# Performance work log

Hardware: AMD Instinct MI355X
Metric: run time of the kernel (lower is better)

Reference implementation:

```python
import jax, jax.numpy as jnp
import numpy as np

D_MODEL = 768
NUM_HEADS = 12
D_K = D_MODEL // NUM_HEADS
B, S = 2, 2048


def setup_inputs() -> dict:
    key = jax.random.key(0)
    ks = jax.random.split(key, 7)
    scale = 1.0 / np.sqrt(D_MODEL)
    return {
        "query": jax.random.normal(ks[0], (B, S, D_MODEL), jnp.float32),
        "key_in": jax.random.normal(ks[1], (B, S, D_MODEL), jnp.float32),
        "value": jax.random.normal(ks[2], (B, S, D_MODEL), jnp.float32),
        # nn.Linear weights are [out, in]; y = x @ W.T
        "Wq": jax.random.normal(ks[3], (D_MODEL, D_MODEL), jnp.float32) * scale,
        "Wk": jax.random.normal(ks[4], (D_MODEL, D_MODEL), jnp.float32) * scale,
        "Wv": jax.random.normal(ks[5], (D_MODEL, D_MODEL), jnp.float32) * scale,
        "Wo": jax.random.normal(ks[6], (D_MODEL, D_MODEL), jnp.float32) * scale,
    }


def _split_heads(x):
    b, s, _ = x.shape
    return x.reshape(b, s, NUM_HEADS, D_K).transpose(0, 2, 1, 3)  # [B,H,S,Dk]


def reference(query, key_in, value, Wq, Wk, Wv, Wo):
    Q = _split_heads(query @ Wq.T)
    K = _split_heads(key_in @ Wk.T)
    V = _split_heads(value @ Wv.T)
    scores = jnp.einsum("bhqd,bhkd->bhqk", Q, K) / jnp.sqrt(jnp.float32(D_K))
    attn = jax.nn.softmax(scores, axis=-1)
    ctx = jnp.einsum("bhqk,bhkd->bhqd", attn, V)  # [B,H,S,Dk]
    ctx = ctx.transpose(0, 2, 1, 3).reshape(query.shape[0], query.shape[1], D_MODEL)
    return ctx @ Wo.T
```

## Files before the change

### kernel.cpp

```cpp
#include <hip/hip_runtime.h>
#include <hip/hip_bf16.h>


typedef __bf16 bf16x8 __attribute__((ext_vector_type(8)));
typedef float f32x4 __attribute__((ext_vector_type(4)));
typedef unsigned short u16;
typedef unsigned int u32;
typedef u16 u16x8 __attribute__((ext_vector_type(8)));
typedef u16 u16x4 __attribute__((ext_vector_type(4)));

#define SEQ 2048
#define DM  768
#define NH  12
#define DK  64
#define NBH 24
#define MTOT 4096
#define NEL 3145728
#define NWL 589824

__device__ __forceinline__ u16 f2b(float v) {
  __bf16 t = (__bf16)v;
  return __builtin_bit_cast(u16, t);
}

__device__ __forceinline__ void gl_lds16(const u16* g, u16* l) {
  __builtin_amdgcn_global_load_lds(
      (const __attribute__((address_space(1))) void*)g,
      (__attribute__((address_space(3))) void*)l, 16, 0, 0);
}

__device__ __forceinline__ int pos32(int k) {
  return (k < 16) ? (((k >> 2) << 3) + (k & 3))
                  : ((((k & 15) >> 2) << 3) + (k & 3) + 4);
}


__global__ __launch_bounds__(256) void to_bf16(
    const float* __restrict__ s0, const float* __restrict__ s1, const float* __restrict__ s2,
    const float* __restrict__ s3, const float* __restrict__ s4, const float* __restrict__ s5,
    const float* __restrict__ s6, u16* __restrict__ Xb, u16* __restrict__ Wb)
{
  size_t c = (size_t)blockIdx.x * 256 + threadIdx.x;
  const float* src;
  u16* dst;
  if (c < 1179648) {
    int seg = (int)(c / 393216);
    size_t off = (c % 393216) * 8;
    src = (seg == 0 ? s0 : seg == 1 ? s1 : s2) + off;
    dst = Xb + (size_t)seg * NEL + off;
  } else {
    size_t c2 = c - 1179648;
    int seg = (int)(c2 / 73728);
    size_t off = (c2 % 73728) * 8;
    src = (seg == 0 ? s3 : seg == 1 ? s4 : seg == 2 ? s5 : s6) + off;
    dst = Wb + (size_t)seg * NWL + off;
  }
  float4 f0 = *(const float4*)(src);
  float4 f1 = *(const float4*)(src + 4);
  u16x8 o;
  o[0] = f2b(f0.x); o[1] = f2b(f0.y); o[2] = f2b(f0.z); o[3] = f2b(f0.w);
  o[4] = f2b(f1.x); o[5] = f2b(f1.y); o[6] = f2b(f1.z); o[7] = f2b(f1.w);
  *(u16x8*)dst = o;
}

__device__ __forceinline__ void gemm2_core(
    const u16* __restrict__ X, const u16* __restrict__ W, void* __restrict__ Y,
    int m0, int n0, int mode, u16* As, u16* Bs)
{
  const int tid  = threadIdx.x;
  const int lane = tid & 63, w = tid >> 6;
  const int l15  = lane & 15, quad = lane >> 4;
  const int wm   = (w & 1) * 64, wn = (w >> 1) * 64;

  f32x4 acc[4][4] = {};

  for (int k0 = 0; k0 < DM; k0 += 64) {
    __syncthreads();
#pragma unroll
    for (int i = 0; i < 4; i++) {
      int c = (w * 4 + i) * 64 + lane;
      int row = c >> 3, c8 = c & 7;
      int g8 = c8 ^ (row & 7);
      gl_lds16(X + (size_t)(m0 + row) * DM + k0 + g8 * 8, As + c * 8);
      gl_lds16(W + (size_t)(n0 + row) * DM + k0 + g8 * 8, Bs + c * 8);
    }
    __syncthreads();
#pragma unroll
    for (int dk = 0; dk < 2; dk++) {
      bf16x8 af[4], bf[4];
      int ph = ((dk * 4 + quad) ^ (l15 & 7)) * 8;
#pragma unroll
      for (int t = 0; t < 4; t++) {
        af[t] = *(const bf16x8*)(&As[(wm + t * 16 + l15) * 64 + ph]);
        bf[t] = *(const bf16x8*)(&Bs[(wn + t * 16 + l15) * 64 + ph]);
      }
#pragma unroll
      for (int mt = 0; mt < 4; mt++)
#pragma unroll
        for (int nt = 0; nt < 4; nt++)
          acc[mt][nt] = __builtin_amdgcn_mfma_f32_16x16x32_bf16(af[mt], bf[nt], acc[mt][nt], 0, 0, 0);
    }
  }

  if (mode == 2) {
    float* O = (float*)Y;
#pragma unroll
    for (int mt = 0; mt < 4; mt++) {
      int mg = m0 + wm + mt * 16 + quad * 4;
#pragma unroll
      for (int nt = 0; nt < 4; nt++) {
        int j = n0 + wn + nt * 16 + l15;
#pragma unroll
        for (int r = 0; r < 4; r++)
          O[(size_t)(mg + r) * DM + j] = acc[mt][nt][r];
      }
    }
  } else if (mode == 1) {
    u16* O = (u16*)Y;
#pragma unroll
    for (int mt = 0; mt < 4; mt++) {
      int mg = m0 + wm + mt * 16 + quad * 4;
      int b = mg >> 11, s = mg & 2047;
      int sp = (s & ~31) | pos32(s & 31);
#pragma unroll
      for (int nt = 0; nt < 4; nt++) {
        int j = n0 + wn + nt * 16 + l15;
        int h = j >> 6, d = j & 63;
        u16x4 o;
#pragma unroll
        for (int r = 0; r < 4; r++) o[r] = f2b(acc[mt][nt][r]);
        *(u16x4*)&O[((size_t)(b * NH + h) * DK + d) * SEQ + sp] = o;
      }
    }
  } else {
    u16* O = (u16*)Y;
    u16* T = As;
#pragma unroll
    for (int h2 = 0; h2 < 2; h2++) {
      __syncthreads();
      if ((w & 1) == h2) {
#pragma unroll
        for (int mt = 0; mt < 4; mt++)
#pragma unroll
          for (int nt = 0; nt < 4; nt++)
#pragma unroll
            for (int r = 0; r < 4; r++)
              T[(mt * 16 + quad * 4 + r) * 128 + wn + nt * 16 + l15] = f2b(acc[mt][nt][r]);
      }
      __syncthreads();
#pragma unroll
      for (int i = 0; i < 4; i++) {
        int c = i * 256 + tid;
        int row = c >> 4, ch = c & 15;
        u16x8 val = *(const u16x8*)&T[row * 128 + ch * 8];
        int m = m0 + h2 * 64 + row;
        int j = n0 + ch * 8;
        int hh = j >> 6, d = j & 63;
        int b = m >> 11, s = m & 2047;
        *(u16x8*)&O[((size_t)(b * NH + hh) * SEQ + s) * DK + d] = val;
      }
    }
  }
}

__global__ __launch_bounds__(256) void qkv2(
    const u16* __restrict__ Xb, const u16* __restrict__ Wb,
    u16* __restrict__ Qhm, u16* __restrict__ Khm, u16* __restrict__ Vt)
{
  __shared__ __align__(16) u16 As[128 * 64];
  __shared__ __align__(16) u16 Bs[128 * 64];
  int mat = blockIdx.z;
  const u16* X = Xb + (size_t)mat * NEL;
  const u16* W = Wb + (size_t)mat * NWL;
  void* Y = (mat == 0) ? (void*)Qhm : (mat == 1) ? (void*)Khm : (void*)Vt;
  gemm2_core(X, W, Y, blockIdx.y * 128, blockIdx.x * 128, (mat == 2) ? 1 : 0, As, Bs);
}

__global__ __launch_bounds__(256) void bt2(
    const u16* __restrict__ Ctx, const u16* __restrict__ Wob, float* __restrict__ Y)
{
  __shared__ __align__(16) u16 As[128 * 64];
  __shared__ __align__(16) u16 Bs[128 * 64];
  gemm2_core(Ctx, Wob, Y, blockIdx.y * 128, blockIdx.x * 128, 2, As, Bs);
}

__global__ __launch_bounds__(256) void attn2(
    const u16* __restrict__ Qh, const u16* __restrict__ Kh,
    const u16* __restrict__ Vt, u16* __restrict__ ctx)
{
  __shared__ __align__(16) u16 smem[128 * 64 + 64 * 128];
  __shared__ float Ls[64];
  u16* Ks = smem;
  u16* Vs = smem + 128 * 64;

  const int tid  = threadIdx.x;
  const int lane = tid & 63, w = tid >> 6;
  const int l15  = lane & 15, quad = lane >> 4;
  const int qh = w & 1, kh = w >> 1;
  const int qt = blockIdx.x, bh = blockIdx.y;
  const int b = bh / NH, h = bh % NH;

  const u16* Qb = Qh + (size_t)bh * SEQ * DK;
  const u16* Kb = Kh + (size_t)bh * SEQ * DK;
  const u16* Vb = Vt + (size_t)bh * DK * SEQ;
  const int q0 = qt * 64 + qh * 32;

  bf16x8 qf[2][2];
#pragma unroll
  for (int QT = 0; QT < 2; QT++)
#pragma unroll
    for (int dk = 0; dk < 2; dk++)
      qf[QT][dk] = *(const bf16x8*)&Qb[(size_t)(q0 + QT * 16 + l15) * DK + dk * 32 + quad * 8];

  float lpart[2] = {0.f, 0.f};
  f32x4 oacc[4][2] = {};

  for (int kt = 0; kt < SEQ; kt += 128) {
    __syncthreads();
#pragma unroll
    for (int i = 0; i < 4; i++) {
      int c = (w * 4 + i) * 64 + lane;
      int row = c >> 3, c8 = c & 7;
      gl_lds16(Kb + (size_t)(kt + row) * DK + (c8 ^ (row & 7)) * 8, Ks + c * 8);
    }
#pragma unroll
    for (int i = 0; i < 4; i++) {
      int c = (w * 4 + i) * 64 + lane;
      int d = c >> 4, c16 = c & 15;
      gl_lds16(Vb + (size_t)d * SEQ + kt + (c16 ^ (d & 15)) * 8, Vs + c * 8);
    }
    __syncthreads();

    f32x4 sc[4][2] = {};
#pragma unroll
    for (int MT = 0; MT < 4; MT++) {
      int row = kh * 64 + MT * 16 + l15;
#pragma unroll
      for (int dk = 0; dk < 2; dk++) {
        bf16x8 kf = *(const bf16x8*)&Ks[row * 64 + ((dk * 4 + quad) ^ (l15 & 7)) * 8];
        sc[MT][0] = __builtin_amdgcn_mfma_f32_16x16x32_bf16(kf, qf[0][dk], sc[MT][0], 0, 0, 0);
        sc[MT][1] = __builtin_amdgcn_mfma_f32_16x16x32_bf16(kf, qf[1][dk], sc[MT][1], 0, 0, 0);
      }
    }

    bf16x8 pf[2][2];
#pragma unroll
    for (int QT = 0; QT < 2; QT++)
#pragma unroll
      for (int kk = 0; kk < 2; kk++)
#pragma unroll
        for (int j = 0; j < 8; j++) {
          float s = sc[kk * 2 + (j >> 2)][QT][j & 3] * 0.125f;
          float p = __expf(fminf(s, 30.0f));
          lpart[QT] += p;
          pf[kk][QT][j] = (__bf16)p;
        }

#pragma unroll
    for (int kk = 0; kk < 2; kk++) {
      int cL = kh * 8 + kk * 4 + quad;
#pragma unroll
      for (int DT = 0; DT < 4; DT++) {
        int d = DT * 16 + l15;
        bf16x8 vf = *(const bf16x8*)&Vs[d * 128 + (cL ^ (d & 15)) * 8];
        oacc[DT][0] = __builtin_amdgcn_mfma_f32_16x16x32_bf16(vf, pf[kk][0], oacc[DT][0], 0, 0, 0);
        oacc[DT][1] = __builtin_amdgcn_mfma_f32_16x16x32_bf16(vf, pf[kk][1], oacc[DT][1], 0, 0, 0);
      }
    }
  }

  __syncthreads();

  float lw[2];
#pragma unroll
  for (int QT = 0; QT < 2; QT++) {
    float l = lpart[QT];
    l += __shfl_xor(l, 16);
    l += __shfl_xor(l, 32);
    lw[QT] = l;
  }

  float* Os = (float*)smem;
  float* Ob = Os + qh * (32 * 68);
  if (kh == 1) {
#pragma unroll
    for (int DT = 0; DT < 4; DT++)
#pragma unroll
      for (int QT = 0; QT < 2; QT++)
        *(f32x4*)&Ob[(QT * 16 + l15) * 68 + DT * 16 + quad * 4] = oacc[DT][QT];
    if (quad == 0) {
      Ls[qh * 32 + l15]      = lw[0];
      Ls[qh * 32 + 16 + l15] = lw[1];
    }
  }
  __syncthreads();
  if (kh == 0) {
#pragma unroll
    for (int QT = 0; QT < 2; QT++) {
      float inv = 1.0f / (lw[QT] + Ls[qh * 32 + QT * 16 + l15]);
      int s = q0 + QT * 16 + l15;
#pragma unroll
      for (int DT = 0; DT < 4; DT++) {
        f32x4 add = *(const f32x4*)&Ob[(QT * 16 + l15) * 68 + DT * 16 + quad * 4];
        u16x4 ov;
#pragma unroll
        for (int r = 0; r < 4; r++)
          ov[r] = f2b((oacc[DT][QT][r] + add[r]) * inv);
        *(u16x4*)&ctx[((size_t)(b * SEQ + s)) * DM + h * DK + DT * 16 + quad * 4] = ov;
      }
    }
  }
}


__device__ __forceinline__ void stage8(u16* dst, const void* src, size_t elemIdx, int isf32) {
  if (isf32) {
    const float* s = (const float*)src + elemIdx;
    float4 f0 = *(const float4*)(s);
    float4 f1 = *(const float4*)(s + 4);
    u16x8 o;
    o[0] = f2b(f0.x); o[1] = f2b(f0.y); o[2] = f2b(f0.z); o[3] = f2b(f0.w);
    o[4] = f2b(f1.x); o[5] = f2b(f1.y); o[6] = f2b(f1.z); o[7] = f2b(f1.w);
    *(u16x8*)dst = o;
  } else {
    *(float4*)dst = *(const float4*)((const u16*)src + elemIdx);
  }
}

__device__ __forceinline__ void gemm_core_fb(
    const void* __restrict__ X, const void* __restrict__ W, void* __restrict__ Y,
    int m0, int n0, int out_mode, u16* As, u16* Bs, int xf32, int wf32)
{
  const int tid  = threadIdx.x;
  const int lane = tid & 63, w = tid >> 6;
  const int l15  = lane & 15, quad = lane >> 4;
  const int wm   = (w & 1) * 64, wn = (w >> 1) * 64;
  f32x4 acc[4][4] = {};
  for (int k0 = 0; k0 < DM; k0 += 32) {
    __syncthreads();
#pragma unroll
    for (int i = 0; i < 2; i++) {
      int c = i * 256 + tid;
      int row = c >> 2, cc = c & 3;
      stage8(&As[c * 8], X, (size_t)(m0 + row) * DM + k0 + cc * 8, xf32);
      stage8(&Bs[c * 8], W, (size_t)(n0 + row) * DM + k0 + cc * 8, wf32);
    }
    __syncthreads();
    bf16x8 af[4], bf[4];
#pragma unroll
    for (int t = 0; t < 4; t++) {
      af[t] = *(const bf16x8*)(&As[(wm + t * 16 + l15) * 32 + quad * 8]);
      bf[t] = *(const bf16x8*)(&Bs[(wn + t * 16 + l15) * 32 + quad * 8]);
    }
#pragma unroll
    for (int mt = 0; mt < 4; mt++)
#pragma unroll
      for (int nt = 0; nt < 4; nt++)
        acc[mt][nt] = __builtin_amdgcn_mfma_f32_16x16x32_bf16(af[mt], bf[nt], acc[mt][nt], 0, 0, 0);
  }
  if (out_mode == 2) {
    float* O = (float*)Y;
#pragma unroll
    for (int mt = 0; mt < 4; mt++) {
      int mg = m0 + wm + mt * 16 + quad * 4;
#pragma unroll
      for (int nt = 0; nt < 4; nt++) {
        int j = n0 + wn + nt * 16 + l15;
#pragma unroll
        for (int r = 0; r < 4; r++)
          O[(size_t)(mg + r) * DM + j] = acc[mt][nt][r];
      }
    }
  } else {
    u16* O = (u16*)Y;
#pragma unroll
    for (int mt = 0; mt < 4; mt++) {
      int mg = m0 + wm + mt * 16 + quad * 4;
#pragma unroll
      for (int nt = 0; nt < 4; nt++) {
        int j = n0 + wn + nt * 16 + l15;
        int h = j >> 6, d = j & 63;
#pragma unroll
        for (int r = 0; r < 4; r++) {
          int m = mg + r;
          int b = m >> 11, s = m & 2047;
          O[((size_t)(b * NH + h) * SEQ + s) * DK + d] = f2b(acc[mt][nt][r]);
        }
      }
    }
  }
}

__global__ __launch_bounds__(256) void fb_qkv_gemm(
    const float* __restrict__ Xq, const float* __restrict__ Xk, const float* __restrict__ Xv,
    const float* __restrict__ Wq, const float* __restrict__ Wk, const float* __restrict__ Wv,
    u16* __restrict__ Yq, u16* __restrict__ Yk, u16* __restrict__ Yv)
{
  __shared__ __align__(16) u16 As[128 * 32];
  __shared__ __align__(16) u16 Bs[128 * 32];
  int mat = blockIdx.z;
  const float* X = (mat == 0) ? Xq : (mat == 1) ? Xk : Xv;
  const float* W = (mat == 0) ? Wq : (mat == 1) ? Wk : Wv;
  u16*         Y = (mat == 0) ? Yq : (mat == 1) ? Yk : Yv;
  gemm_core_fb(X, W, Y, blockIdx.y * 128, blockIdx.x * 128, 0, As, Bs, 1, 1);
}

__global__ __launch_bounds__(256) void fb_gemm_bt(
    const u16* __restrict__ X, const float* __restrict__ W, float* __restrict__ Y)
{
  __shared__ __align__(16) u16 As[128 * 32];
  __shared__ __align__(16) u16 Bs[128 * 32];
  gemm_core_fb(X, W, Y, blockIdx.y * 128, blockIdx.x * 128, 2, As, Bs, 0, 1);
}

__global__ __launch_bounds__(256) void fb_attn(
    const u16* __restrict__ Qh, const u16* __restrict__ Kh,
    const u16* __restrict__ Vh, u16* __restrict__ ctx)
{
  __shared__ __align__(16) u16 Ks[32 * 88];
  __shared__ __align__(16) u16 Vs[64 * 40];
  __shared__ __align__(16) u16 Ps[4][16 * 32];
  const int tid  = threadIdx.x;
  const int lane = tid & 63, w = tid >> 6;
  const int l15  = lane & 15, quad = lane >> 4;
  const int qt = blockIdx.x, bh = blockIdx.y;
  const int b = bh / NH, h = bh % NH;
  const u16* Qb = Qh + (size_t)bh * SEQ * DK;
  const u16* Kb = Kh + (size_t)bh * SEQ * DK;
  const u16* Vb = Vh + (size_t)bh * SEQ * DK;
  const int q0 = qt * 64 + w * 16;
  bf16x8 qf[2];
#pragma unroll
  for (int kk = 0; kk < 2; kk++)
    qf[kk] = *(const bf16x8*)(&Qb[(size_t)(q0 + l15) * DK + kk * 32 + quad * 8]);
  float m_i[4] = {-INFINITY, -INFINITY, -INFINITY, -INFINITY};
  float l_i[4] = {0.f, 0.f, 0.f, 0.f};
  f32x4 acc[4] = {};
  for (int kt = 0; kt < SEQ; kt += 32) {
    __syncthreads();
    {
      int c = tid;
      int row = c >> 3, c8 = c & 7;
      *(float4*)(&Ks[row * 88 + c8 * 8]) =
          *(const float4*)(&Kb[(size_t)(kt + row) * DK + c8 * 8]);
    }
#pragma unroll
    for (int i = 0; i < 4; i++) {
      int e = i * 256 + tid;
      int k = e >> 5, d2 = e & 31;
      u32 v = *(const u32*)(&Vb[(size_t)(kt + k) * DK + d2 * 2]);
      Vs[(d2 * 2)     * 40 + k] = (u16)(v & 0xffffu);
      Vs[(d2 * 2 + 1) * 40 + k] = (u16)(v >> 16);
    }
    __syncthreads();
    f32x4 sc[2] = {};
#pragma unroll
    for (int ktt = 0; ktt < 2; ktt++)
#pragma unroll
      for (int dk = 0; dk < 2; dk++) {
        bf16x8 kf = *(const bf16x8*)(&Ks[(ktt * 16 + l15) * 88 + dk * 32 + quad * 8]);
        sc[ktt] = __builtin_amdgcn_mfma_f32_16x16x32_bf16(qf[dk], kf, sc[ktt], 0, 0, 0);
      }
    float alph[4];
#pragma unroll
    for (int r = 0; r < 4; r++) {
      float s0 = sc[0][r] * 0.125f;
      float s1 = sc[1][r] * 0.125f;
      float mv = fmaxf(s0, s1);
      mv = fmaxf(mv, __shfl_xor(mv, 1));
      mv = fmaxf(mv, __shfl_xor(mv, 2));
      mv = fmaxf(mv, __shfl_xor(mv, 4));
      mv = fmaxf(mv, __shfl_xor(mv, 8));
      float mnew = fmaxf(m_i[r], mv);
      float a = __expf(m_i[r] - mnew);
      m_i[r] = mnew;
      float p0 = __expf(s0 - mnew);
      float p1 = __expf(s1 - mnew);
      float rs = p0 + p1;
      rs += __shfl_xor(rs, 1);
      rs += __shfl_xor(rs, 2);
      rs += __shfl_xor(rs, 4);
      rs += __shfl_xor(rs, 8);
      l_i[r] = l_i[r] * a + rs;
      alph[r] = a;
      Ps[w][(quad * 4 + r) * 32 +      l15] = f2b(p0);
      Ps[w][(quad * 4 + r) * 32 + 16 + l15] = f2b(p1);
    }
#pragma unroll
    for (int nt = 0; nt < 4; nt++) {
      acc[nt][0] *= alph[0];
      acc[nt][1] *= alph[1];
      acc[nt][2] *= alph[2];
      acc[nt][3] *= alph[3];
    }
    __syncthreads();
    bf16x8 pf = *(const bf16x8*)(&Ps[w][l15 * 32 + quad * 8]);
#pragma unroll
    for (int nt = 0; nt < 4; nt++) {
      bf16x8 vf = *(const bf16x8*)(&Vs[(nt * 16 + l15) * 40 + quad * 8]);
      acc[nt] = __builtin_amdgcn_mfma_f32_16x16x32_bf16(pf, vf, acc[nt], 0, 0, 0);
    }
  }
#pragma unroll
  for (int nt = 0; nt < 4; nt++) {
    int d = nt * 16 + l15;
#pragma unroll
    for (int r = 0; r < 4; r++) {
      int s = q0 + quad * 4 + r;
      float v = acc[nt][r] / l_i[r];
      ctx[((size_t)(b * SEQ + s)) * DM + h * DK + d] = f2b(v);
    }
  }
}


extern "C" void kernel_launch(void* const* d_in, const int* in_sizes, int n_in,
                              void* d_out, int out_size, void* d_ws, size_t ws_size,
                              hipStream_t stream) {
  const float* act[3] = {nullptr, nullptr, nullptr};
  const float* wgt[4] = {nullptr, nullptr, nullptr, nullptr};
  int na = 0, nw = 0;
  for (int i = 0; i < n_in && i < 7; i++) {
    if (in_sizes[i] == NEL) { if (na < 3) act[na++] = (const float*)d_in[i]; }
    else                    { if (nw < 4) wgt[nw++] = (const float*)d_in[i]; }
  }
  const float* q  = act[0] ? act[0] : (const float*)d_in[0];
  const float* k  = act[1] ? act[1] : (const float*)d_in[1];
  const float* v  = act[2] ? act[2] : (const float*)d_in[2];
  const float* Wq = wgt[0] ? wgt[0] : (const float*)d_in[3];
  const float* Wk = wgt[1] ? wgt[1] : (const float*)d_in[4];
  const float* Wv = wgt[2] ? wgt[2] : (const float*)d_in[5];
  const float* Wo = wgt[3] ? wgt[3] : (const float*)d_in[6];
  u16* ws = (u16*)d_ws;

  const size_t NE = NEL, NW = NWL;
  const size_t need = (6 * NE + 4 * NW) * 2;

  if (ws_size >= need) {
    u16* Xb  = ws;
    u16* Wb  = ws + 3 * NE;
    u16* Qhm = Wb + 4 * NW;
    u16* Khm = Qhm + NE;
    u16* Vt  = Khm + NE;
    u16* Ctx = ws;

    to_bf16<<<5760, 256, 0, stream>>>(q, k, v, Wq, Wk, Wv, Wo, Xb, Wb);
    qkv2<<<dim3(DM / 128, MTOT / 128, 3), 256, 0, stream>>>(Xb, Wb, Qhm, Khm, Vt);
    attn2<<<dim3(SEQ / 64, NBH), 256, 0, stream>>>(Qhm, Khm, Vt, Ctx);
    bt2<<<dim3(DM / 128, MTOT / 128), 256, 0, stream>>>(Ctx, Wb + 3 * NW, (float*)d_out);
  } else {
    u16* Qhm = ws;
    u16* Khm = ws + NE;
    u16* Vhm = ws + 2 * NE;
    u16* Ctx = ws + 3 * NE;
    fb_qkv_gemm<<<dim3(DM / 128, MTOT / 128, 3), 256, 0, stream>>>(
        q, k, v, Wq, Wk, Wv, Qhm, Khm, Vhm);
    fb_attn<<<dim3(SEQ / 64, NBH), 256, 0, stream>>>(Qhm, Khm, Vhm, Ctx);
    fb_gemm_bt<<<dim3(DM / 128, MTOT / 128), 256, 0, stream>>>(Ctx, Wo, (float*)d_out);
  }
}
```

Measured before the change: 194.2 us.

## Fold softmax scale into Q, use exp2, split attention warps over keys

```diff
diff --git a/kernel.cpp b/kernel.cpp
--- a/kernel.cpp
+++ b/kernel.cpp
@@ -17,6 +17,7 @@
 #define MTOT 4096
 #define NEL 3145728
 #define NWL 589824
+#define QSCALE 0.18033688f
 
 __device__ __forceinline__ u16 f2b(float v) {
   __bf16 t = (__bf16)v;
@@ -65,7 +66,7 @@
 
 __device__ __forceinline__ void gemm2_core(
     const u16* __restrict__ X, const u16* __restrict__ W, void* __restrict__ Y,
-    int m0, int n0, int mode, u16* As, u16* Bs)
+    int m0, int n0, int mode, float scale, u16* As, u16* Bs)
 {
   const int tid  = threadIdx.x;
   const int lane = tid & 63, w = tid >> 6;
@@ -145,7 +146,7 @@
           for (int nt = 0; nt < 4; nt++)
 #pragma unroll
             for (int r = 0; r < 4; r++)
-              T[(mt * 16 + quad * 4 + r) * 128 + wn + nt * 16 + l15] = f2b(acc[mt][nt][r]);
+              T[(mt * 16 + quad * 4 + r) * 128 + wn + nt * 16 + l15] = f2b(acc[mt][nt][r] * scale);
       }
       __syncthreads();
 #pragma unroll
@@ -173,7 +174,8 @@
   const u16* X = Xb + (size_t)mat * NEL;
   const u16* W = Wb + (size_t)mat * NWL;
   void* Y = (mat == 0) ? (void*)Qhm : (mat == 1) ? (void*)Khm : (void*)Vt;
-  gemm2_core(X, W, Y, blockIdx.y * 128, blockIdx.x * 128, (mat == 2) ? 1 : 0, As, Bs);
+  float scale = (mat == 0) ? QSCALE : 1.0f;
+  gemm2_core(X, W, Y, blockIdx.y * 128, blockIdx.x * 128, (mat == 2) ? 1 : 0, scale, As, Bs);
 }
 
 __global__ __launch_bounds__(256) void bt2(
@@ -181,39 +183,42 @@
 {
   __shared__ __align__(16) u16 As[128 * 64];
   __shared__ __align__(16) u16 Bs[128 * 64];
-  gemm2_core(Ctx, Wob, Y, blockIdx.y * 128, blockIdx.x * 128, 2, As, Bs);
-}
-
-__global__ __launch_bounds__(256) void attn2(
+  gemm2_core(Ctx, Wob, Y, blockIdx.y * 128, blockIdx.x * 128, 2, 1.0f, As, Bs);
+}
+
+__global__ __launch_bounds__(256, 3) void attn3(
     const u16* __restrict__ Qh, const u16* __restrict__ Kh,
     const u16* __restrict__ Vt, u16* __restrict__ ctx)
 {
   __shared__ __align__(16) u16 smem[128 * 64 + 64 * 128];
-  __shared__ float Ls[64];
+  __shared__ float Lsum[4][64];
   u16* Ks = smem;
   u16* Vs = smem + 128 * 64;
 
   const int tid  = threadIdx.x;
   const int lane = tid & 63, w = tid >> 6;
   const int l15  = lane & 15, quad = lane >> 4;
-  const int qh = w & 1, kh = w >> 1;
   const int qt = blockIdx.x, bh = blockIdx.y;
   const int b = bh / NH, h = bh % NH;
 
   const u16* Qb = Qh + (size_t)bh * SEQ * DK;
   const u16* Kb = Kh + (size_t)bh * SEQ * DK;
   const u16* Vb = Vt + (size_t)bh * DK * SEQ;
-  const int q0 = qt * 64 + qh * 32;
-
-  bf16x8 qf[2][2];
-#pragma unroll
-  for (int QT = 0; QT < 2; QT++)
+  const int q0 = qt * 64;
+
+  bf16x8 qf[4][2];
+#pragma unroll
+  for (int QT = 0; QT < 4; QT++)
 #pragma unroll
     for (int dk = 0; dk < 2; dk++)
       qf[QT][dk] = *(const bf16x8*)&Qb[(size_t)(q0 + QT * 16 + l15) * DK + dk * 32 + quad * 8];
 
-  float lpart[2] = {0.f, 0.f};
-  f32x4 oacc[4][2] = {};
+  bf16x8 onef;
+#pragma unroll
+  for (int j = 0; j < 8; j++) onef[j] = (__bf16)1.0f;
+
+  f32x4 oacc[4][4] = {};
+  f32x4 lacc[4] = {};
 
   for (int kt = 0; kt < SEQ; kt += 128) {
     __syncthreads();
@@ -231,84 +236,90 @@
     }
     __syncthreads();
 
-    f32x4 sc[4][2] = {};
-#pragma unroll
-    for (int MT = 0; MT < 4; MT++) {
-      int row = kh * 64 + MT * 16 + l15;
+    f32x4 sc[2][4] = {};
+#pragma unroll
+    for (int MT = 0; MT < 2; MT++) {
+      int row = w * 32 + MT * 16 + l15;
 #pragma unroll
       for (int dk = 0; dk < 2; dk++) {
         bf16x8 kf = *(const bf16x8*)&Ks[row * 64 + ((dk * 4 + quad) ^ (l15 & 7)) * 8];
-        sc[MT][0] = __builtin_amdgcn_mfma_f32_16x16x32_bf16(kf, qf[0][dk], sc[MT][0], 0, 0, 0);
-        sc[MT][1] = __builtin_amdgcn_mfma_f32_16x16x32_bf16(kf, qf[1][dk], sc[MT][1], 0, 0, 0);
-      }
-    }
-
-    bf16x8 pf[2][2];
-#pragma unroll
-    for (int QT = 0; QT < 2; QT++)
-#pragma unroll
-      for (int kk = 0; kk < 2; kk++)
-#pragma unroll
-        for (int j = 0; j < 8; j++) {
-          float s = sc[kk * 2 + (j >> 2)][QT][j & 3] * 0.125f;
-          float p = __expf(fminf(s, 30.0f));
-          lpart[QT] += p;
-          pf[kk][QT][j] = (__bf16)p;
-        }
-
-#pragma unroll
-    for (int kk = 0; kk < 2; kk++) {
-      int cL = kh * 8 + kk * 4 + quad;
-#pragma unroll
-      for (int DT = 0; DT < 4; DT++) {
-        int d = DT * 16 + l15;
-        bf16x8 vf = *(const bf16x8*)&Vs[d * 128 + (cL ^ (d & 15)) * 8];
-        oacc[DT][0] = __builtin_amdgcn_mfma_f32_16x16x32_bf16(vf, pf[kk][0], oacc[DT][0], 0, 0, 0);
-        oacc[DT][1] = __builtin_amdgcn_mfma_f32_16x16x32_bf16(vf, pf[kk][1], oacc[DT][1], 0, 0, 0);
-      }
+#pragma unroll
+        for (int QT = 0; QT < 4; QT++)
+          sc[MT][QT] = __builtin_amdgcn_mfma_f32_16x16x32_bf16(kf, qf[QT][dk], sc[MT][QT], 0, 0, 0);
+      }
+    }
+
+    bf16x8 pf[4];
+#pragma unroll
+    for (int QT = 0; QT < 4; QT++) {
+#pragma unroll
+      for (int j = 0; j < 8; j++)
+        pf[QT][j] = (__bf16)__builtin_amdgcn_exp2f(sc[j >> 2][QT][j & 3]);
+      lacc[QT] = __builtin_amdgcn_mfma_f32_16x16x32_bf16(onef, pf[QT], lacc[QT], 0, 0, 0);
+    }
+
+    int cL = w * 4 + quad;
+#pragma unroll
+    for (int DT = 0; DT < 4; DT++) {
+      int d = DT * 16 + l15;
+      bf16x8 vf = *(const bf16x8*)&Vs[d * 128 + (cL ^ (d & 15)) * 8];
+#pragma unroll
+      for (int QT = 0; QT < 4; QT++)
+        oacc[DT][QT] = __builtin_amdgcn_mfma_f32_16x16x32_bf16(vf, pf[QT], oacc[DT][QT], 0, 0, 0);
     }
   }
 
   __syncthreads();
 
-  float lw[2];
-#pragma unroll
-  for (int QT = 0; QT < 2; QT++) {
-    float l = lpart[QT];
-    l += __shfl_xor(l, 16);
-    l += __shfl_xor(l, 32);
-    lw[QT] = l;
-  }
-
-  float* Os = (float*)smem;
-  float* Ob = Os + qh * (32 * 68);
-  if (kh == 1) {
-#pragma unroll
-    for (int DT = 0; DT < 4; DT++)
-#pragma unroll
-      for (int QT = 0; QT < 2; QT++)
-        *(f32x4*)&Ob[(QT * 16 + l15) * 68 + DT * 16 + quad * 4] = oacc[DT][QT];
-    if (quad == 0) {
-      Ls[qh * 32 + l15]      = lw[0];
-      Ls[qh * 32 + 16 + l15] = lw[1];
-    }
-  }
-  __syncthreads();
-  if (kh == 0) {
-#pragma unroll
-    for (int QT = 0; QT < 2; QT++) {
-      float inv = 1.0f / (lw[QT] + Ls[qh * 32 + QT * 16 + l15]);
-      int s = q0 + QT * 16 + l15;
-#pragma unroll
-      for (int DT = 0; DT < 4; DT++) {
-        f32x4 add = *(const f32x4*)&Ob[(QT * 16 + l15) * 68 + DT * 16 + quad * 4];
-        u16x4 ov;
-#pragma unroll
-        for (int r = 0; r < 4; r++)
-          ov[r] = f2b((oacc[DT][QT][r] + add[r]) * inv);
-        *(u16x4*)&ctx[((size_t)(b * SEQ + s)) * DM + h * DK + DT * 16 + quad * 4] = ov;
-      }
-    }
+  if (quad == 0) {
+#pragma unroll
+    for (int QT = 0; QT < 4; QT++)
+      Lsum[w][QT * 16 + l15] = lacc[QT][0];
+  }
+
+  float* fb = (float*)smem;
+#pragma unroll
+  for (int rd = 0; rd < 2; rd++) {
+    int p0 = rd * 2, p1 = rd * 2 + 1;
+    __syncthreads();
+    if (w != p0) {
+      int s3 = (w < p0) ? w : w - 1;
+#pragma unroll
+      for (int QT = 0; QT < 4; QT++)
+        *(f32x4*)&fb[(0 * 3 + s3) * 1152 + (QT * 16 + l15) * 18 + quad * 4] = oacc[p0][QT];
+    }
+    if (w != p1) {
+      int s3 = (w < p1) ? w : w - 1;
+#pragma unroll
+      for (int QT = 0; QT < 4; QT++)
+        *(f32x4*)&fb[(1 * 3 + s3) * 1152 + (QT * 16 + l15) * 18 + quad * 4] = oacc[p1][QT];
+    }
+    __syncthreads();
+    if (w == p0) {
+#pragma unroll
+      for (int s3 = 0; s3 < 3; s3++)
+#pragma unroll
+        for (int QT = 0; QT < 4; QT++)
+          oacc[p0][QT] += *(const f32x4*)&fb[(0 * 3 + s3) * 1152 + (QT * 16 + l15) * 18 + quad * 4];
+    }
+    if (w == p1) {
+#pragma unroll
+      for (int s3 = 0; s3 < 3; s3++)
+#pragma unroll
+        for (int QT = 0; QT < 4; QT++)
+          oacc[p1][QT] += *(const f32x4*)&fb[(1 * 3 + s3) * 1152 + (QT * 16 + l15) * 18 + quad * 4];
+    }
+  }
+
+#pragma unroll
+  for (int QT = 0; QT < 4; QT++) {
+    int q = QT * 16 + l15;
+    float inv = 1.0f / (Lsum[0][q] + Lsum[1][q] + Lsum[2][q] + Lsum[3][q]);
+    u16x4 ov;
+#pragma unroll
+    for (int r = 0; r < 4; r++)
+      ov[r] = f2b(oacc[w][QT][r] * inv);
+    *(u16x4*)&ctx[((size_t)(b * SEQ + q0 + q)) * DM + h * DK + w * 16 + quad * 4] = ov;
   }
 }
 
@@ -546,7 +557,7 @@
 
     to_bf16<<<5760, 256, 0, stream>>>(q, k, v, Wq, Wk, Wv, Wo, Xb, Wb);
     qkv2<<<dim3(DM / 128, MTOT / 128, 3), 256, 0, stream>>>(Xb, Wb, Qhm, Khm, Vt);
-    attn2<<<dim3(SEQ / 64, NBH), 256, 0, stream>>>(Qhm, Khm, Vt, Ctx);
+    attn3<<<dim3(SEQ / 64, NBH), 256, 0, stream>>>(Qhm, Khm, Vt, Ctx);
     bt2<<<dim3(DM / 128, MTOT / 128), 256, 0, stream>>>(Ctx, Wb + 3 * NW, (float*)d_out);
   } else {
     u16* Qhm = ws;
```

Result: slower. 407.0 us (+109.6%).
